# Kernel optimization log

Measured on AMD Instinct MI355X. Metric: run time of the kernel, lower is better.

The kernel has to match this reference:

```python
import jax, jax.numpy as jnp
import numpy as np

D_MODEL = 1024
NUM_HEADS = 16
B, S = 4, 2048


def setup_inputs() -> dict:
    key = jax.random.key(0)
    ks = jax.random.split(key, 9)
    sc = 1.0 / np.sqrt(D_MODEL)
    return {
        "inputs": jax.random.normal(ks[0], (B, S, D_MODEL), dtype=jnp.float32),
        "Wq": jax.random.normal(ks[1], (D_MODEL, D_MODEL), dtype=jnp.float32) * sc,
        "bq": jax.random.normal(ks[2], (D_MODEL,), dtype=jnp.float32) * 0.02,
        "Wk": jax.random.normal(ks[3], (D_MODEL, D_MODEL), dtype=jnp.float32) * sc,
        "bk": jax.random.normal(ks[4], (D_MODEL,), dtype=jnp.float32) * 0.02,
        "Wv": jax.random.normal(ks[5], (D_MODEL, D_MODEL), dtype=jnp.float32) * sc,
        "bv": jax.random.normal(ks[6], (D_MODEL,), dtype=jnp.float32) * 0.02,
        "Wo": jax.random.normal(ks[7], (D_MODEL, D_MODEL), dtype=jnp.float32) * sc,
        "bo": jax.random.normal(ks[8], (D_MODEL,), dtype=jnp.float32) * 0.02,
    }


def reference(inputs, Wq, bq, Wk, bk, Wv, bv, Wo, bo):
    H = NUM_HEADS
    b, s, d = inputs.shape
    hd = d // H  # head dim for q, k, v (all equal here)

    # Linear projections, then split into heads: [B, H, S, hd]
    def split_heads(x):
        return x.reshape(b, s, H, hd).transpose(0, 2, 1, 3)

    q = split_heads(inputs @ Wq + bq)
    k = split_heads(inputs @ Wk + bk)
    v = split_heads(inputs @ Wv + bv)

    # Scaled dot-product attention per head (batched over B, H)
    scores = jnp.einsum("bhqd,bhkd->bhqk", q, k) / jnp.sqrt(jnp.asarray(hd, dtype=q.dtype))
    causal = jnp.tril(jnp.ones((s, s), dtype=bool))
    scores = jnp.where(causal[None, None], scores, jnp.asarray(-jnp.inf, dtype=scores.dtype))
    attn = jax.nn.softmax(scores, axis=-1)
    ctx = jnp.einsum("bhqk,bhkd->bhqd", attn, v)  # [B, H, S, hd]

    # Concatenate heads and final projection
    concat = ctx.transpose(0, 2, 1, 3).reshape(b, s, d)
    return concat @ Wo + bo
```

## Files before the change

kernel.cpp:

```cpp
#include <hip/hip_runtime.h>
#include <hip/hip_bf16.h>
#include <math.h>

typedef __attribute__((ext_vector_type(8))) short short8;
typedef __attribute__((ext_vector_type(4))) float floatx4;
typedef __attribute__((ext_vector_type(16))) float floatx16;

#define D_MODEL 1024
#define NHEAD   16
#define HD      64
#define BATCH   4
#define SEQ     2048
#define M_TOT   (BATCH * SEQ)

__device__ __forceinline__ unsigned short f2bf(float f) {
  unsigned int u = __builtin_bit_cast(unsigned int, f);
  u += 0x7FFFu + ((u >> 16) & 1u);
  return (unsigned short)(u >> 16);
}

__device__ __forceinline__ unsigned pk2(float a, float b) {
  unsigned r;
  asm("v_cvt_pk_bf16_f32 %0, %1, %2" : "=v"(r) : "v"(a), "v"(b));
  return r;
}

__device__ __forceinline__ void gl_lds16(const void* g, void* l) {
  __builtin_amdgcn_global_load_lds((__attribute__((address_space(1))) void*)g,
                                   (__attribute__((address_space(3))) void*)l,
                                   16, 0, 0);
}

__device__ __forceinline__ int aswz(int r) { return (r ^ (r >> 3)) & 7; }

__global__ __launch_bounds__(256) void cvt_x_kernel(const float* __restrict__ X,
                                                    unsigned short* __restrict__ Xb) {
  int i = blockIdx.x * 256 + threadIdx.x;
  float4 v = reinterpret_cast<const float4*>(X)[i];
  ushort4 o;
  o.x = f2bf(v.x); o.y = f2bf(v.y); o.z = f2bf(v.z); o.w = f2bf(v.w);
  reinterpret_cast<ushort4*>(Xb)[i] = o;
}

__global__ __launch_bounds__(256) void cvt_wt_kernel(const float* __restrict__ W0,
                                                     const float* __restrict__ W1,
                                                     const float* __restrict__ W2,
                                                     const float* __restrict__ W3,
                                                     unsigned short* __restrict__ T0,
                                                     unsigned short* __restrict__ T1,
                                                     unsigned short* __restrict__ T2,
                                                     unsigned short* __restrict__ T3) {
  const float* W;
  unsigned short* T;
  switch (blockIdx.z) {
    case 0: W = W0; T = T0; break;
    case 1: W = W1; T = T1; break;
    case 2: W = W2; T = T2; break;
    default: W = W3; T = T3; break;
  }
  __shared__ unsigned short tile[64][65];
  int n0 = blockIdx.x * 64, k0 = blockIdx.y * 64;
#pragma unroll
  for (int i = 0; i < 16; ++i) {
    int e = threadIdx.x + i * 256;
    int r = e >> 6, c = e & 63;
    tile[r][c] = f2bf(W[(size_t)(k0 + r) * D_MODEL + n0 + c]);
  }
  __syncthreads();
#pragma unroll
  for (int i = 0; i < 16; ++i) {
    int e = threadIdx.x + i * 256;
    int r = e >> 6, c = e & 63;
    T[(size_t)(n0 + r) * D_MODEL + k0 + c] = tile[c][r];
  }
}

__global__ __launch_bounds__(256) void qkv_gemm_kernel(
    const unsigned short* __restrict__ Xb,
    const unsigned short* __restrict__ WqT, const unsigned short* __restrict__ WkT,
    const unsigned short* __restrict__ WvT,
    const float* __restrict__ bq, const float* __restrict__ bk, const float* __restrict__ bv,
    unsigned short* __restrict__ Qo, unsigned short* __restrict__ Ko,
    unsigned short* __restrict__ Vo) {
  const unsigned short* Bt;
  const float* bias;
  unsigned short* Out;
  float scale;
  if (blockIdx.z == 0)      { Bt = WqT; bias = bq; Out = Qo; scale = 0.18033688f; }
  else if (blockIdx.z == 1) { Bt = WkT; bias = bk; Out = Ko; scale = 1.0f; }
  else                      { Bt = WvT; bias = bv; Out = Vo; scale = 1.0f; }

  __shared__ unsigned short As[128 * 64];
  __shared__ unsigned short Bs[128 * 64];

  int m0 = blockIdx.x * 128, n0 = blockIdx.y * 128;
  int tid = threadIdx.x;
  int lane = tid & 63;
  int w = tid >> 6;
  int wr = (w >> 1) * 64, wc = (w & 1) * 64;
  int l15 = lane & 15, lg = lane >> 4;
  int lr8 = lane >> 3, lc8 = lane & 7;

  floatx4 acc[4][4];
#pragma unroll
  for (int mi = 0; mi < 4; ++mi)
#pragma unroll
    for (int ni = 0; ni < 4; ++ni)
#pragma unroll
      for (int e = 0; e < 4; ++e) acc[mi][ni][e] = 0.0f;

  for (int kt = 0; kt < D_MODEL / 64; ++kt) {
    int k0 = kt * 64;
#pragma unroll
    for (int i = 0; i < 4; ++i) {
      int c = w + i * 4;
      int r = c * 8 + lr8;
      int blk = lc8 ^ (r & 7);
      gl_lds16(&Xb[(size_t)(m0 + r) * D_MODEL + k0 + blk * 8], &As[c * 512]);
      gl_lds16(&Bt[(size_t)(n0 + r) * D_MODEL + k0 + blk * 8], &Bs[c * 512]);
    }
    __syncthreads();
#pragma unroll
    for (int kk = 0; kk < 2; ++kk) {
      short8 af[4], bf[4];
#pragma unroll
      for (int mi = 0; mi < 4; ++mi) {
        int row = wr + mi * 16 + l15;
        int col = (kk * 32 + lg * 8) ^ ((row & 7) << 3);
        af[mi] = *reinterpret_cast<const short8*>(&As[row * 64 + col]);
      }
#pragma unroll
      for (int ni = 0; ni < 4; ++ni) {
        int row = wc + ni * 16 + l15;
        int col = (kk * 32 + lg * 8) ^ ((row & 7) << 3);
        bf[ni] = *reinterpret_cast<const short8*>(&Bs[row * 64 + col]);
      }
#pragma unroll
      for (int mi = 0; mi < 4; ++mi)
#pragma unroll
        for (int ni = 0; ni < 4; ++ni)
          acc[mi][ni] =
              __builtin_amdgcn_mfma_f32_16x16x32_bf16(af[mi], bf[ni], acc[mi][ni], 0, 0, 0);
    }
    __syncthreads();
  }

  bool vout = (blockIdx.z == 2);
#pragma unroll
  for (int mi = 0; mi < 4; ++mi)
#pragma unroll
    for (int ni = 0; ni < 4; ++ni) {
      int n = n0 + wc + ni * 16 + l15;
      float bia = bias[n];
      int h = n >> 6, d = n & 63;
#pragma unroll
      for (int r = 0; r < 4; ++r) {
        int m = m0 + wr + mi * 16 + lg * 4 + r;
        int b = m >> 11, s = m & 2047;
        float val = (acc[mi][ni][r] + bia) * scale;
        size_t idx;
        if (vout)
          idx = (((size_t)(b * NHEAD + h)) * HD + d) * SEQ + s;
        else
          idx = (((size_t)(b * NHEAD + h)) * SEQ + s) * HD + d;
        Out[idx] = f2bf(val);
      }
    }
}

__global__ __launch_bounds__(256) void attn_kernel(const unsigned short* __restrict__ Q,
                                                   const unsigned short* __restrict__ K,
                                                   const unsigned short* __restrict__ Vt,
                                                   unsigned short* __restrict__ ctx) {
  __shared__ unsigned short Ks[2][64 * 64];
  __shared__ unsigned short Vs[2][64 * 64];

  int bh = blockIdx.y;
  int tid = threadIdx.x;
  int lane = tid & 63;
  int w = tid >> 6;
  int l31 = lane & 31;
  int hi = lane >> 5;
  int lr8 = lane >> 3, lc8 = lane & 7;

  const unsigned short* Qb = Q + (size_t)bh * SEQ * HD;
  const unsigned short* Kb = K + (size_t)bh * SEQ * HD;
  const unsigned short* Vb = Vt + (size_t)bh * HD * SEQ;
  int b = bh >> 4, h = bh & 15;

  for (int ph = 0; ph < 2; ++ph) {
    int qt = (ph == 0) ? (int)blockIdx.x : 15 - (int)blockIdx.x;
    int q0 = qt * 128;
    int myq = q0 + w * 32 + l31;

    short8 qf[4];
#pragma unroll
    for (int kc = 0; kc < 4; ++kc)
      qf[kc] = *reinterpret_cast<const short8*>(&Qb[(size_t)myq * HD + kc * 16 + hi * 8]);

    floatx16 oacc[2];
#pragma unroll
    for (int db = 0; db < 2; ++db)
#pragma unroll
      for (int r = 0; r < 16; ++r) oacc[db][r] = 0.0f;
    float mrow = -INFINITY;
    float lrow = 0.0f;

    int nt = 2 * qt + 2;

#pragma unroll
    for (int i = 0; i < 2; ++i) {
      int c = w + i * 4;
      int r = c * 8 + lr8;
      int blk = lc8 ^ aswz(r);
      gl_lds16(&Kb[(size_t)r * HD + blk * 8], &Ks[0][c * 512]);
      gl_lds16(&Vb[(size_t)r * SEQ + blk * 8], &Vs[0][c * 512]);
    }
    __syncthreads();

    for (int t = 0; t < nt; ++t) {
      int buf = t & 1;
      if (t + 1 < nt) {
        int kb1 = (t + 1) * 64;
        const unsigned short* kg = Kb + (size_t)kb1 * HD;
        const unsigned short* vg = Vb + kb1;
#pragma unroll
        for (int i = 0; i < 2; ++i) {
          int c = w + i * 4;
          int r = c * 8 + lr8;
          int blk = lc8 ^ aswz(r);
          gl_lds16(&kg[(size_t)r * HD + blk * 8], &Ks[buf ^ 1][c * 512]);
          gl_lds16(&vg[(size_t)r * SEQ + blk * 8], &Vs[buf ^ 1][c * 512]);
        }
      }

      floatx16 sfT[2];
#pragma unroll
      for (int kb = 0; kb < 2; ++kb) {
#pragma unroll
        for (int r = 0; r < 16; ++r) sfT[kb][r] = 0.0f;
#pragma unroll
        for (int kc = 0; kc < 4; ++kc) {
          int row = kb * 32 + l31;
          int col = (kc * 16 + hi * 8) ^ (aswz(row) << 3);
          short8 kf = *reinterpret_cast<const short8*>(&Ks[buf][row * 64 + col]);
          sfT[kb] = __builtin_amdgcn_mfma_f32_32x32x16_bf16(kf, qf[kc], sfT[kb], 0, 0, 0);
        }
      }

      if (t >= nt - 2) {
        int kb0 = t * 64;
#pragma unroll
        for (int kb = 0; kb < 2; ++kb)
#pragma unroll
          for (int r = 0; r < 16; ++r) {
            int key = kb0 + kb * 32 + (r & 3) + 8 * (r >> 2) + 4 * hi;
            if (key > myq) sfT[kb][r] = -INFINITY;
          }
      }

      float tm[16];
#pragma unroll
      for (int r = 0; r < 16; ++r) tm[r] = fmaxf(sfT[0][r], sfT[1][r]);
#pragma unroll
      for (int s = 8; s > 0; s >>= 1)
#pragma unroll
        for (int r = 0; r < 8; ++r)
          if (r < s) tm[r] = fmaxf(tm[r], tm[r + s]);
      float pm = fmaxf(tm[0], __shfl_xor(tm[0], 32));

      if (__any(pm > mrow + 11.5f)) {
        float nm = fmaxf(mrow, pm);
        float sc = exp2f(mrow - nm);
        mrow = nm;
        lrow *= sc;
        int base32 = lane & 32;
#pragma unroll
        for (int r = 0; r < 16; ++r) {
          int q31 = (r & 3) + 8 * (r >> 2) + 4 * hi;
          float sr = __shfl(sc, base32 + q31);
          oacc[0][r] *= sr;
          oacc[1][r] *= sr;
        }
      }

      float ts = 0.0f;
#pragma unroll
      for (int kb = 0; kb < 2; ++kb)
#pragma unroll
        for (int r = 0; r < 16; ++r) {
          float pe = exp2f(sfT[kb][r] - mrow);
          sfT[kb][r] = pe;
          ts += pe;
        }
      ts += __shfl_xor(ts, 32);
      lrow += ts;

#pragma unroll
      for (int kb = 0; kb < 2; ++kb) {
        unsigned D[8];
#pragma unroll
        for (int m = 0; m < 8; ++m) D[m] = pk2(sfT[kb][2 * m], sfT[kb][2 * m + 1]);
#pragma unroll
        for (int c = 0; c < 2; ++c) {
          unsigned send0 = hi ? D[4 * c] : D[4 * c + 2];
          unsigned send1 = hi ? D[4 * c + 1] : D[4 * c + 3];
          unsigned recv0 = (unsigned)__shfl_xor((int)send0, 32);
          unsigned recv1 = (unsigned)__shfl_xor((int)send1, 32);
          uint4 u;
          u.x = hi ? recv0 : D[4 * c];
          u.y = hi ? recv1 : D[4 * c + 1];
          u.z = hi ? D[4 * c + 2] : recv0;
          u.w = hi ? D[4 * c + 3] : recv1;
          short8 pa = __builtin_bit_cast(short8, u);
          int kc = kb * 2 + c;
#pragma unroll
          for (int db = 0; db < 2; ++db) {
            int row = db * 32 + l31;
            int col = (kc * 16 + hi * 8) ^ (aswz(row) << 3);
            short8 vf = *reinterpret_cast<const short8*>(&Vs[buf][row * 64 + col]);
            oacc[db] = __builtin_amdgcn_mfma_f32_32x32x16_bf16(pa, vf, oacc[db], 0, 0, 0);
          }
        }
      }
      __syncthreads();
    }

    int base32 = lane & 32;
    float lrowD[16];
#pragma unroll
    for (int r = 0; r < 16; ++r) {
      int q31 = (r & 3) + 8 * (r >> 2) + 4 * hi;
      lrowD[r] = __shfl(lrow, base32 + q31);
    }
#pragma unroll
    for (int db = 0; db < 2; ++db) {
      int d = db * 32 + l31;
#pragma unroll
      for (int r = 0; r < 16; ++r) {
        int qr = q0 + w * 32 + (r & 3) + 8 * (r >> 2) + 4 * hi;
        float val = oacc[db][r] / lrowD[r];
        ctx[((size_t)(b * SEQ + qr)) * D_MODEL + h * HD + d] = f2bf(val);
      }
    }
    __syncthreads();
  }
}

__global__ __launch_bounds__(256) void out_gemm_kernel(const unsigned short* __restrict__ A,
                                                       const unsigned short* __restrict__ Bt,
                                                       const float* __restrict__ bias,
                                                       float* __restrict__ Out) {
  __shared__ unsigned short As[128 * 64];
  __shared__ unsigned short Bs[128 * 64];

  int m0 = blockIdx.x * 128, n0 = blockIdx.y * 128;
  int tid = threadIdx.x;
  int lane = tid & 63;
  int w = tid >> 6;
  int wr = (w >> 1) * 64, wc = (w & 1) * 64;
  int l15 = lane & 15, lg = lane >> 4;
  int lr8 = lane >> 3, lc8 = lane & 7;

  floatx4 acc[4][4];
#pragma unroll
  for (int mi = 0; mi < 4; ++mi)
#pragma unroll
    for (int ni = 0; ni < 4; ++ni)
#pragma unroll
      for (int e = 0; e < 4; ++e) acc[mi][ni][e] = 0.0f;

  for (int kt = 0; kt < D_MODEL / 64; ++kt) {
    int k0 = kt * 64;
#pragma unroll
    for (int i = 0; i < 4; ++i) {
      int c = w + i * 4;
      int r = c * 8 + lr8;
      int blk = lc8 ^ (r & 7);
      gl_lds16(&A[(size_t)(m0 + r) * D_MODEL + k0 + blk * 8], &As[c * 512]);
      gl_lds16(&Bt[(size_t)(n0 + r) * D_MODEL + k0 + blk * 8], &Bs[c * 512]);
    }
    __syncthreads();
#pragma unroll
    for (int kk = 0; kk < 2; ++kk) {
      short8 af[4], bf[4];
#pragma unroll
      for (int mi = 0; mi < 4; ++mi) {
        int row = wr + mi * 16 + l15;
        int col = (kk * 32 + lg * 8) ^ ((row & 7) << 3);
        af[mi] = *reinterpret_cast<const short8*>(&As[row * 64 + col]);
      }
#pragma unroll
      for (int ni = 0; ni < 4; ++ni) {
        int row = wc + ni * 16 + l15;
        int col = (kk * 32 + lg * 8) ^ ((row & 7) << 3);
        bf[ni] = *reinterpret_cast<const short8*>(&Bs[row * 64 + col]);
      }
#pragma unroll
      for (int mi = 0; mi < 4; ++mi)
#pragma unroll
        for (int ni = 0; ni < 4; ++ni)
          acc[mi][ni] =
              __builtin_amdgcn_mfma_f32_16x16x32_bf16(af[mi], bf[ni], acc[mi][ni], 0, 0, 0);
    }
    __syncthreads();
  }

#pragma unroll
  for (int mi = 0; mi < 4; ++mi)
#pragma unroll
    for (int ni = 0; ni < 4; ++ni) {
      int n = n0 + wc + ni * 16 + l15;
      float bia = bias[n];
#pragma unroll
      for (int r = 0; r < 4; ++r) {
        int m = m0 + wr + mi * 16 + lg * 4 + r;
        Out[(size_t)m * D_MODEL + n] = acc[mi][ni][r] + bia;
      }
    }
}

extern "C" void kernel_launch(void* const* d_in, const int* in_sizes, int n_in,
                              void* d_out, int out_size, void* d_ws, size_t ws_size,
                              hipStream_t stream) {
  const float* X  = (const float*)d_in[0];
  const float* Wq = (const float*)d_in[1];
  const float* bq = (const float*)d_in[2];
  const float* Wk = (const float*)d_in[3];
  const float* bk = (const float*)d_in[4];
  const float* Wv = (const float*)d_in[5];
  const float* bv = (const float*)d_in[6];
  const float* Wo = (const float*)d_in[7];
  const float* bo = (const float*)d_in[8];
  float* out = (float*)d_out;

  char* ws = (char*)d_ws;
  const size_t MB = 1024 * 1024;
  unsigned short* Xb   = (unsigned short*)(ws);
  unsigned short* WqT  = (unsigned short*)(ws + 16 * MB);
  unsigned short* WkT  = (unsigned short*)(ws + 18 * MB);
  unsigned short* WvT  = (unsigned short*)(ws + 20 * MB);
  unsigned short* WoT  = (unsigned short*)(ws + 22 * MB);
  unsigned short* Qw   = (unsigned short*)(ws + 24 * MB);
  unsigned short* Kw   = (unsigned short*)(ws + 40 * MB);
  unsigned short* Vtw  = (unsigned short*)(ws + 56 * MB);
  unsigned short* Ctx  = (unsigned short*)(ws + 72 * MB);

  cvt_x_kernel<<<(M_TOT * D_MODEL / 4) / 256, 256, 0, stream>>>(X, Xb);
  cvt_wt_kernel<<<dim3(16, 16, 4), 256, 0, stream>>>(Wq, Wk, Wv, Wo, WqT, WkT, WvT, WoT);
  qkv_gemm_kernel<<<dim3(M_TOT / 128, D_MODEL / 128, 3), 256, 0, stream>>>(
      Xb, WqT, WkT, WvT, bq, bk, bv, Qw, Kw, Vtw);
  attn_kernel<<<dim3(8, BATCH * NHEAD), 256, 0, stream>>>(Qw, Kw, Vtw, Ctx);
  out_gemm_kernel<<<dim3(M_TOT / 128, D_MODEL / 128), 256, 0, stream>>>(Ctx, WoT, bo, out);
}
```

Measured before the change: 297.5 us.

## Double-buffer GEMM LDS tiles, raise MFMA priority in attention, flatten max reduction

Both projection GEMMs now use two LDS buffers and issue the global-to-LDS loads for the next K tile before computing the current one. This overlaps memory latency with MFMA work and removes one barrier per iteration. In the attention loop, s_setprio is raised around the two MFMA sections so waves doing matrix math get issue priority, and the row-max reduction becomes a flatter tree of fmax calls. LDS use in the GEMMs doubles to 64KB per block, which may lower occupancy.

```diff
diff --git a/kernel.cpp b/kernel.cpp
--- a/kernel.cpp
+++ b/kernel.cpp
@@ -90,8 +90,8 @@
   else if (blockIdx.z == 1) { Bt = WkT; bias = bk; Out = Ko; scale = 1.0f; }
   else                      { Bt = WvT; bias = bv; Out = Vo; scale = 1.0f; }
 
-  __shared__ unsigned short As[128 * 64];
-  __shared__ unsigned short Bs[128 * 64];
+  __shared__ unsigned short As[2][128 * 64];
+  __shared__ unsigned short Bs[2][128 * 64];
 
   int m0 = blockIdx.x * 128, n0 = blockIdx.y * 128;
   int tid = threadIdx.x;
@@ -109,17 +109,24 @@
 #pragma unroll
       for (int e = 0; e < 4; ++e) acc[mi][ni][e] = 0.0f;
 
-  for (int kt = 0; kt < D_MODEL / 64; ++kt) {
-    int k0 = kt * 64;
+  auto stage = [&](int bufi, int k0) {
 #pragma unroll
     for (int i = 0; i < 4; ++i) {
       int c = w + i * 4;
       int r = c * 8 + lr8;
       int blk = lc8 ^ (r & 7);
-      gl_lds16(&Xb[(size_t)(m0 + r) * D_MODEL + k0 + blk * 8], &As[c * 512]);
-      gl_lds16(&Bt[(size_t)(n0 + r) * D_MODEL + k0 + blk * 8], &Bs[c * 512]);
-    }
-    __syncthreads();
+      gl_lds16(&Xb[(size_t)(m0 + r) * D_MODEL + k0 + blk * 8], &As[bufi][c * 512]);
+      gl_lds16(&Bt[(size_t)(n0 + r) * D_MODEL + k0 + blk * 8], &Bs[bufi][c * 512]);
+    }
+  };
+
+  stage(0, 0);
+  __syncthreads();
+
+  const int NT = D_MODEL / 64;
+  for (int kt = 0; kt < NT; ++kt) {
+    int cur = kt & 1;
+    if (kt + 1 < NT) stage(cur ^ 1, (kt + 1) * 64);
 #pragma unroll
     for (int kk = 0; kk < 2; ++kk) {
       short8 af[4], bf[4];
@@ -127,13 +134,13 @@
       for (int mi = 0; mi < 4; ++mi) {
         int row = wr + mi * 16 + l15;
         int col = (kk * 32 + lg * 8) ^ ((row & 7) << 3);
-        af[mi] = *reinterpret_cast<const short8*>(&As[row * 64 + col]);
+        af[mi] = *reinterpret_cast<const short8*>(&As[cur][row * 64 + col]);
       }
 #pragma unroll
       for (int ni = 0; ni < 4; ++ni) {
         int row = wc + ni * 16 + l15;
         int col = (kk * 32 + lg * 8) ^ ((row & 7) << 3);
-        bf[ni] = *reinterpret_cast<const short8*>(&Bs[row * 64 + col]);
+        bf[ni] = *reinterpret_cast<const short8*>(&Bs[cur][row * 64 + col]);
       }
 #pragma unroll
       for (int mi = 0; mi < 4; ++mi)
@@ -235,6 +242,7 @@
       }
 
       floatx16 sfT[2];
+      __builtin_amdgcn_s_setprio(1);
 #pragma unroll
       for (int kb = 0; kb < 2; ++kb) {
 #pragma unroll
@@ -247,6 +255,7 @@
           sfT[kb] = __builtin_amdgcn_mfma_f32_32x32x16_bf16(kf, qf[kc], sfT[kb], 0, 0, 0);
         }
       }
+      __builtin_amdgcn_s_setprio(0);
 
       if (t >= nt - 2) {
         int kb0 = t * 64;
@@ -262,12 +271,15 @@
       float tm[16];
 #pragma unroll
       for (int r = 0; r < 16; ++r) tm[r] = fmaxf(sfT[0][r], sfT[1][r]);
-#pragma unroll
-      for (int s = 8; s > 0; s >>= 1)
-#pragma unroll
-        for (int r = 0; r < 8; ++r)
-          if (r < s) tm[r] = fmaxf(tm[r], tm[r + s]);
-      float pm = fmaxf(tm[0], __shfl_xor(tm[0], 32));
+      float a0 = fmaxf(fmaxf(tm[0], tm[1]), tm[2]);
+      float a1 = fmaxf(fmaxf(tm[3], tm[4]), tm[5]);
+      float a2 = fmaxf(fmaxf(tm[6], tm[7]), tm[8]);
+      float a3 = fmaxf(fmaxf(tm[9], tm[10]), tm[11]);
+      float a4 = fmaxf(fmaxf(tm[12], tm[13]), tm[14]);
+      float a5 = fmaxf(fmaxf(a0, a1), a2);
+      float a6 = fmaxf(fmaxf(a3, a4), tm[15]);
+      float pm0 = fmaxf(a5, a6);
+      float pm = fmaxf(pm0, __shfl_xor(pm0, 32));
 
       if (__any(pm > mrow + 11.5f)) {
         float nm = fmaxf(mrow, pm);
@@ -296,6 +308,7 @@
       ts += __shfl_xor(ts, 32);
       lrow += ts;
 
+      __builtin_amdgcn_s_setprio(1);
 #pragma unroll
       for (int kb = 0; kb < 2; ++kb) {
         unsigned D[8];
@@ -323,6 +336,7 @@
           }
         }
       }
+      __builtin_amdgcn_s_setprio(0);
       __syncthreads();
     }
 
@@ -351,8 +365,8 @@
                                                        const unsigned short* __restrict__ Bt,
                                                        const float* __restrict__ bias,
                                                        float* __restrict__ Out) {
-  __shared__ unsigned short As[128 * 64];
-  __shared__ unsigned short Bs[128 * 64];
+  __shared__ unsigned short As[2][128 * 64];
+  __shared__ unsigned short Bs[2][128 * 64];
 
   int m0 = blockIdx.x * 128, n0 = blockIdx.y * 128;
   int tid = threadIdx.x;
@@ -370,17 +384,24 @@
 #pragma unroll
       for (int e = 0; e < 4; ++e) acc[mi][ni][e] = 0.0f;
 
-  for (int kt = 0; kt < D_MODEL / 64; ++kt) {
-    int k0 = kt * 64;
+  auto stage = [&](int bufi, int k0) {
 #pragma unroll
     for (int i = 0; i < 4; ++i) {
       int c = w + i * 4;
       int r = c * 8 + lr8;
       int blk = lc8 ^ (r & 7);
-      gl_lds16(&A[(size_t)(m0 + r) * D_MODEL + k0 + blk * 8], &As[c * 512]);
-      gl_lds16(&Bt[(size_t)(n0 + r) * D_MODEL + k0 + blk * 8], &Bs[c * 512]);
-    }
-    __syncthreads();
+      gl_lds16(&A[(size_t)(m0 + r) * D_MODEL + k0 + blk * 8], &As[bufi][c * 512]);
+      gl_lds16(&Bt[(size_t)(n0 + r) * D_MODEL + k0 + blk * 8], &Bs[bufi][c * 512]);
+    }
+  };
+
+  stage(0, 0);
+  __syncthreads();
+
+  const int NT = D_MODEL / 64;
+  for (int kt = 0; kt < NT; ++kt) {
+    int cur = kt & 1;
+    if (kt + 1 < NT) stage(cur ^ 1, (kt + 1) * 64);
 #pragma unroll
     for (int kk = 0; kk < 2; ++kk) {
       short8 af[4], bf[4];
@@ -388,13 +409,13 @@
       for (int mi = 0; mi < 4; ++mi) {
         int row = wr + mi * 16 + l15;
         int col = (kk * 32 + lg * 8) ^ ((row & 7) << 3);
-        af[mi] = *reinterpret_cast<const short8*>(&As[row * 64 + col]);
+        af[mi] = *reinterpret_cast<const short8*>(&As[cur][row * 64 + col]);
       }
 #pragma unroll
       for (int ni = 0; ni < 4; ++ni) {
         int row = wc + ni * 16 + l15;
         int col = (kk * 32 + lg * 8) ^ ((row & 7) << 3);
-        bf[ni] = *reinterpret_cast<const short8*>(&Bs[row * 64 + col]);
+        bf[ni] = *reinterpret_cast<const short8*>(&Bs[cur][row * 64 + col]);
       }
 #pragma unroll
       for (int mi = 0; mi < 4; ++mi)
```

Measured after the change: 302.9 us. About the same (+1.8%).
